# Kernel tuning notes

Measured on AMD Instinct MI355X. Metric: run time of the kernel, lower is better.

## Reference

```python
import jax, jax.numpy as jnp
import numpy as np

N = 50000
E = 800000
HEADS = 4
CH = 64
NEG_SLOPE = 0.2


def _ln(x, g, b, eps=1e-5):
    m = x.mean(-1, keepdims=True)
    v = ((x - m) ** 2).mean(-1, keepdims=True)
    return (x - m) / jnp.sqrt(v + eps) * g + b


def _gat_conv(x, src, dst, W, att_src, att_dst, bias, heads, ch, concat):
    """PyG-style GATConv (self-loops already appended to src/dst)."""
    n = x.shape[0]
    h = (x @ W).reshape(n, heads, ch)                 # [N,H,C]
    a_s = (h * att_src).sum(-1)                        # [N,H]
    a_d = (h * att_dst).sum(-1)                        # [N,H]
    e = jax.nn.leaky_relu(a_s[src] + a_d[dst], NEG_SLOPE)   # [E',H]
    emax = jax.ops.segment_max(e, dst, num_segments=n)      # every node has a self-loop
    ex = jnp.exp(e - emax[dst])
    denom = jax.ops.segment_sum(ex, dst, num_segments=n)
    alpha = ex / (denom[dst] + 1e-16)                  # [E',H]
    out = jax.ops.segment_sum(alpha[:, :, None] * h[src], dst, num_segments=n)  # [N,H,C]
    out = out.reshape(n, heads * ch) if concat else out.mean(axis=1)
    return out + bias


def setup_inputs() -> dict:
    key = jax.random.key(0)
    ks = jax.random.split(key, 32)
    s = 0.05
    inp = {
        "positions": jax.random.normal(ks[0], (N, 3), jnp.float32),
        "degrees": jax.random.uniform(ks[1], (N,), jnp.float32),
        "traffic_info": jax.random.normal(ks[2], (5,), jnp.float32),
        "edge_index": jax.random.randint(ks[3], (2, E), 0, N, jnp.int64),
        # node_encoder: Linear(4,32) + LayerNorm(32)
        "enc_w": jax.random.normal(ks[4], (4, 32), jnp.float32) * s,
        "enc_b": jnp.zeros((32,), jnp.float32),
        "enc_g": jnp.ones((32,), jnp.float32),
        "enc_be": jnp.zeros((32,), jnp.float32),
        # gat1: in=32, out=64, heads=4, concat
        "gat1_w": jax.random.normal(ks[5], (32, HEADS * CH), jnp.float32) * s,
        "gat1_as": jax.random.normal(ks[6], (HEADS, CH), jnp.float32) * s,
        "gat1_ad": jax.random.normal(ks[7], (HEADS, CH), jnp.float32) * s,
        "gat1_b": jnp.zeros((HEADS * CH,), jnp.float32),
        "n1_g": jnp.ones((HEADS * CH,), jnp.float32),
        "n1_b": jnp.zeros((HEADS * CH,), jnp.float32),
        # residual proj Linear(32,64)
        "proj_w": jax.random.normal(ks[8], (32, CH), jnp.float32) * s,
        "proj_b": jnp.zeros((CH,), jnp.float32),
        # gat2: in=256, out=64, heads=1, mean
        "gat2_w": jax.random.normal(ks[9], (HEADS * CH, CH), jnp.float32) * s,
        "gat2_as": jax.random.normal(ks[10], (1, CH), jnp.float32) * s,
        "gat2_ad": jax.random.normal(ks[11], (1, CH), jnp.float32) * s,
        "gat2_b": jnp.zeros((CH,), jnp.float32),
        "n2_g": jnp.ones((CH,), jnp.float32),
        "n2_b": jnp.zeros((CH,), jnp.float32),
        # traffic_encoder Linear(5,32)+LN
        "tr_w": jax.random.normal(ks[12], (5, 32), jnp.float32) * s,
        "tr_b": jnp.zeros((32,), jnp.float32),
        "tr_g": jnp.ones((32,), jnp.float32),
        "tr_be": jnp.zeros((32,), jnp.float32),
        # fusion Linear(96,256)+LN
        "fu_w": jax.random.normal(ks[13], (CH + 32, 256), jnp.float32) * s,
        "fu_b": jnp.zeros((256,), jnp.float32),
        "fu_g": jnp.ones((256,), jnp.float32),
        "fu_be": jnp.zeros((256,), jnp.float32),
    }
    return inp


def reference(positions, degrees, traffic_info, enc_w, enc_b, enc_g, enc_be,
              gat1_w, gat1_as, gat1_ad, gat1_b, n1_g, n1_b, proj_w, proj_b,
              gat2_w, gat2_as, gat2_ad, gat2_b, n2_g, n2_b,
              tr_w, tr_b, tr_g, tr_be, fu_w, fu_b, fu_g, fu_be, edge_index):
    n = positions.shape[0]
    loops = jnp.arange(n, dtype=edge_index.dtype)
    src = jnp.concatenate([edge_index[0], loops])
    dst = jnp.concatenate([edge_index[1], loops])
    # node encoder (dropout in eval mode => identity)
    nf = jnp.concatenate([positions, degrees[:, None]], axis=-1)       # [N,4]
    x = _ln(jax.nn.relu(nf @ enc_w + enc_b), enc_g, enc_be)           # [N,32]
    identity = x @ proj_w + proj_b                                     # [N,64]
    h = _gat_conv(x, src, dst, gat1_w, gat1_as, gat1_ad, gat1_b, HEADS, CH, True)
    h = jax.nn.elu(_ln(h, n1_g, n1_b))                                 # [N,256]
    h = _gat_conv(h, src, dst, gat2_w, gat2_as, gat2_ad, gat2_b, 1, CH, False)
    h = jax.nn.elu(_ln(h, n2_g, n2_b) + identity)                      # [N,64]
    pooled = h.mean(axis=0, keepdims=True)                             # [1,64]
    tf = _ln(jax.nn.relu(traffic_info @ tr_w + tr_b), tr_g, tr_be)[None, :]  # [1,32]
    comb = jnp.concatenate([pooled, tf], axis=-1)                      # [1,96]
    return _ln(jax.nn.relu(comb @ fu_w + fu_b), fu_g, fu_be)           # [1,256]
```

## Files before the change

### kernel.cpp

```cpp
#include <hip/hip_runtime.h>


#define NN 50000
#define EE 800000
#define DMAX 32
#define OVCAP 8192
#define NBLK2 3136
#define ENC_BLOCKS 196
#define NB 196
#define LCAP 20
#define BCAP 8192
#define SPCAP 131072
#define ACHUNK 2048
#define A_BLOCKS 391
#define BSTRIDE 16

typedef unsigned short u16;
typedef unsigned int u32;
typedef __attribute__((ext_vector_type(8))) short bf16x8;
typedef __attribute__((ext_vector_type(4))) float f32x4;

__device__ __forceinline__ float b2f(u16 h) { return __uint_as_float(((u32)h) << 16); }
__device__ __forceinline__ float blo(u32 w) { return __uint_as_float(w << 16); }
__device__ __forceinline__ float bhi(u32 w) { return __uint_as_float(w & 0xFFFF0000u); }
__device__ __forceinline__ u16 f2b(float f) {
    u32 u = __float_as_uint(f);
    u32 r = u + 0x7FFFu + ((u >> 16) & 1u);
    return (u16)(r >> 16);
}
__device__ __forceinline__ int hswz(int row, int u16off) {
    return (row * 256 + u16off) ^ ((row & 7) << 3);
}

template <int BF>
__device__ __forceinline__ float ldf(const void* p, int i) {
    if (BF) return b2f(reinterpret_cast<const u16*>(p)[i]);
    return reinterpret_cast<const float*>(p)[i];
}
template <int I64>
__device__ __forceinline__ int ldidx(const void* p, int i) {
    if (I64) return (int)reinterpret_cast<const long long*>(p)[i];
    return reinterpret_cast<const int*>(p)[i];
}

__device__ __forceinline__ int det_bf(const void* enc_g) {
    return *reinterpret_cast<const u32*>(enc_g) == 0x3F803F80u;
}
__device__ __forceinline__ int det_i64(const void* eidx) {
    const int* e = reinterpret_cast<const int*>(eidx);
    return (e[1] == 0 && e[3] == 0 && e[5] == 0);
}

__device__ __forceinline__ float lrelu(float x) { return x > 0.f ? x : 0.2f * x; }
__device__ __forceinline__ float elu(float x) { return x > 0.f ? x : (__expf(x) - 1.f); }
__device__ __forceinline__ float wsum64(float v) {
#pragma unroll
    for (int off = 1; off < 64; off <<= 1) v += __shfl_xor(v, off, 64);
    return v;
}

template <int BF>
__device__ void swz_body(const void* w1, u16* w1p, int base, int stride) {
    for (int D = base; D < 8192; D += stride) {
        int r = D & 7, ln = (D >> 3) & 63, t = (D >> 9) & 3, h = (D >> 11) & 3;
        int k = (ln >> 4) * 8 + r, c = h * 64 + t * 16 + (ln & 15);
        w1p[D] = BF ? reinterpret_cast<const u16*>(w1)[k * 256 + c]
                    : f2b(reinterpret_cast<const float*>(w1)[k * 256 + c]);
    }
}
template <int BF>
__device__ void swzp_body(const void* pw, u16* pwp, int base, int stride) {
    for (int D = base; D < 2048; D += stride) {
        int r = D & 7, ln = (D >> 3) & 63, t = (D >> 9) & 3;
        int k = (ln >> 4) * 8 + r, c = t * 16 + (ln & 15);
        pwp[D] = BF ? reinterpret_cast<const u16*>(pw)[k * 64 + c]
                    : f2b(reinterpret_cast<const float*>(pw)[k * 64 + c]);
    }
}
template <int BF>
__device__ void swz2s_body(const void* w2, u16* w2p, int base, int stride) {
    for (int D = base; D < 16384; D += stride) {
        int r = D & 7, ln = (D >> 3) & 63, ks = (D >> 9) & 7, t = (D >> 12) & 3;
        int k = ks * 32 + (ln >> 4) * 8 + r, c = t * 16 + (ln & 15);
        w2p[D] = BF ? reinterpret_cast<const u16*>(w2)[k * 64 + c]
                    : f2b(reinterpret_cast<const float*>(w2)[k * 64 + c]);
    }
}
template <int BF>
__device__ void swz2_dots(const void* w2, const void* as2v, const void* ad2v, float* was2p,
                          float* wad2p) {
    int k = threadIdx.x;
    float ss = 0.f, dd = 0.f;
    for (int c = 0; c < 64; c++) {
        float wv = ldf<BF>(w2, k * 64 + c);
        ss = fmaf(wv, ldf<BF>(as2v, c), ss);
        dd = fmaf(wv, ldf<BF>(ad2v, c), dd);
    }
    was2p[k] = ss;
    wad2p[k] = dd;
}
__global__ __launch_bounds__(256) void k_swz(const void* w1, const void* pw, const void* w2,
                                             const void* as2v, const void* ad2v,
                                             const void* enc_g, u16* w1p, u16* pwp, u16* w2p,
                                             float* was2p, float* wad2p) {
    int bf = det_bf(enc_g);
    int bid = blockIdx.x;
    if (bid < 16) {
        int base = bid * 256 + threadIdx.x, stride = 16 * 256;
        if (bf) {
            swz_body<1>(w1, w1p, base, stride);
            swzp_body<1>(pw, pwp, base, stride);
            swz2s_body<1>(w2, w2p, base, stride);
        } else {
            swz_body<0>(w1, w1p, base, stride);
            swzp_body<0>(pw, pwp, base, stride);
            swz2s_body<0>(w2, w2p, base, stride);
        }
    } else {
        if (bf) swz2_dots<1>(w2, as2v, ad2v, was2p, wad2p);
        else swz2_dots<0>(w2, as2v, ad2v, was2p, wad2p);
    }
}

template <int I64>
__device__ void binA_body(const void* eidx, u32* bucket, int* bcnt, int* spill, int* scnt, int sb,
                          u32* lbin, int* bc, int* bbase) {
    for (int b = threadIdx.x; b < NB; b += 256) bc[b] = 0;
    __syncthreads();
    int base = sb * ACHUNK;
#pragma unroll
    for (int j = 0; j < 8; j++) {
        int e = base + j * 256 + threadIdx.x;
        if (e < EE) {
            int s = ldidx<I64>(eidx, e);
            int d = ldidx<I64>(eidx, EE + e);
            int b = d >> 8;
            int p = atomicAdd(&bc[b], 1);
            if (p < LCAP) {
                lbin[b * LCAP + p] = ((u32)(d & 255) << 16) | (u32)s;
            } else {
                int o = atomicAdd(scnt, 1);
                if (o < SPCAP) { spill[2 * o] = d; spill[2 * o + 1] = s; }
            }
        }
    }
    __syncthreads();
    for (int b = threadIdx.x; b < NB; b += 256) {
        int c = bc[b];
        if (c > LCAP) c = LCAP;
        bc[b] = c;
        int cr = (c + 15) & ~15;
        bbase[b] = cr > 0 ? atomicAdd(&bcnt[b * BSTRIDE], cr) : 0;
    }
    __syncthreads();
    int wave = threadIdx.x >> 6, lane = threadIdx.x & 63;
    for (int b = wave; b < NB; b += 4) {
        int c = bc[b], bs = bbase[b];
        int cr = (c + 15) & ~15;
        for (int i = lane; i < cr; i += 64) {
            int pos = bs + i;
            u32 w = (i < c) ? lbin[b * LCAP + i] : 0xFFFF0000u;
            if (pos < BCAP) {
                bucket[(size_t)b * BCAP + pos] = w;
            } else if (i < c) {
                int o = atomicAdd(scnt, 1);
                if (o < SPCAP) {
                    spill[2 * o] = (b << 8) | (int)(w >> 16);
                    spill[2 * o + 1] = (int)(w & 0xFFFFu);
                }
            }
        }
    }
}

template <int BF>
__device__ void enc_body(const void* pos, const void* deg, const void* enc_w, const void* enc_b,
                         const void* enc_g, const void* enc_be, const u16* pwp,
                         const void* proj_b, u16* xo, float* identity, float* a_s1, float* a_d1,
                         const float (*vs)[32], const float (*vd)[32], u32* aggE, int b) {
    int tid = threadIdx.x;
    int n = b * 256 + tid;
    int valid = n < NN;
    float v[32];
#pragma unroll
    for (int c = 0; c < 32; c++) v[c] = 0.f;
    if (valid) {
        float f0 = ldf<BF>(pos, n * 3 + 0), f1 = ldf<BF>(pos, n * 3 + 1);
        float f2 = ldf<BF>(pos, n * 3 + 2), f3 = ldf<BF>(deg, n);
        float s = 0.f, q = 0.f;
#pragma unroll
        for (int c = 0; c < 32; c++) {
            float a = ldf<BF>(enc_b, c) + f0 * ldf<BF>(enc_w, c) + f1 * ldf<BF>(enc_w, 32 + c) +
                      f2 * ldf<BF>(enc_w, 64 + c) + f3 * ldf<BF>(enc_w, 96 + c);
            a = fmaxf(a, 0.f);
            v[c] = a;
            s += a;
            q += a * a;
        }
        float m = s * (1.f / 32.f);
        float rstd = rsqrtf(q * (1.f / 32.f) - m * m + 1e-5f);
#pragma unroll
        for (int c = 0; c < 32; c++) {
            v[c] = (v[c] - m) * rstd * ldf<BF>(enc_g, c) + ldf<BF>(enc_be, c);
            xo[n * 32 + c] = f2b(v[c]);
        }
#pragma unroll
        for (int h = 0; h < 4; h++) {
            float ss = 0.f, dd = 0.f;
#pragma unroll
            for (int k = 0; k < 32; k++) {
                ss = fmaf(v[k], vs[h][k], ss);
                dd = fmaf(v[k], vd[h][k], dd);
            }
            a_s1[n * 4 + h] = ss;
            a_d1[n * 4 + h] = dd;
        }
    }
#pragma unroll
    for (int p = 0; p < 16; p++)
        aggE[tid * 16 + p] = valid ? ((u32)f2b(v[2 * p]) | ((u32)f2b(v[2 * p + 1]) << 16)) : 0u;
    __syncthreads();

    int wave = tid >> 6, lane = tid & 63;
    bf16x8 bf0 = __builtin_bit_cast(bf16x8, *reinterpret_cast<const uint4*>(pwp + ((0 * 64 + lane)) * 8));
    bf16x8 bf1 = __builtin_bit_cast(bf16x8, *reinterpret_cast<const uint4*>(pwp + ((1 * 64 + lane)) * 8));
    bf16x8 bf2 = __builtin_bit_cast(bf16x8, *reinterpret_cast<const uint4*>(pwp + ((2 * 64 + lane)) * 8));
    bf16x8 bf3 = __builtin_bit_cast(bf16x8, *reinterpret_cast<const uint4*>(pwp + ((3 * 64 + lane)) * 8));
    int col = lane & 15;
    float pb0 = ldf<BF>(proj_b, 0 * 16 + col);
    float pb1 = ldf<BF>(proj_b, 1 * 16 + col);
    float pb2 = ldf<BF>(proj_b, 2 * 16 + col);
    float pb3 = ldf<BF>(proj_b, 3 * 16 + col);
    f32x4 z = {0.f, 0.f, 0.f, 0.f};
#pragma unroll
    for (int s = 0; s < 4; s++) {
        int rowbase = wave * 64 + s * 16;
        uint4 au = *reinterpret_cast<const uint4*>(aggE + (rowbase + col) * 16 + (lane >> 4) * 4);
        bf16x8 af = __builtin_bit_cast(bf16x8, au);
        f32x4 c0 = __builtin_amdgcn_mfma_f32_16x16x32_bf16(af, bf0, z, 0, 0, 0);
        f32x4 c1 = __builtin_amdgcn_mfma_f32_16x16x32_bf16(af, bf1, z, 0, 0, 0);
        f32x4 c2 = __builtin_amdgcn_mfma_f32_16x16x32_bf16(af, bf2, z, 0, 0, 0);
        f32x4 c3 = __builtin_amdgcn_mfma_f32_16x16x32_bf16(af, bf3, z, 0, 0, 0);
        int rb2 = (lane >> 4) * 4;
#pragma unroll
        for (int rr = 0; rr < 4; rr++) {
            int node = b * 256 + rowbase + rb2 + rr;
            if (node < NN) {
                identity[(size_t)node * 64 + 0 * 16 + col] = c0[rr] + pb0;
                identity[(size_t)node * 64 + 1 * 16 + col] = c1[rr] + pb1;
                identity[(size_t)node * 64 + 2 * 16 + col] = c2[rr] + pb2;
                identity[(size_t)node * 64 + 3 * 16 + col] = c3[rr] + pb3;
            }
        }
    }
}
template <int BF>
__device__ void enc_pre(const void* w1, const void* asv, const void* adv, float (*vs)[32],
                        float (*vd)[32]) {
    int t = threadIdx.x;
    int h = (t >> 5) & 3, k = t & 31;
    const void* att = (t >> 7) ? adv : asv;
    float s = 0.f;
    for (int c = 0; c < 64; c++)
        s = fmaf(ldf<BF>(w1, k * 256 + h * 64 + c), ldf<BF>(att, h * 64 + c), s);
    if (t >> 7) vd[h][k] = s;
    else vs[h][k] = s;
}
__global__ __launch_bounds__(256) void kAS_bin_enc(
    const void* pos, const void* deg, const void* enc_w, const void* enc_b, const void* enc_g,
    const void* enc_be, const void* proj_b, const void* w1, const void* asv,
    const void* adv, const void* eidx, u16* xo, float* identity, float* a_s1, float* a_d1,
    u32* bucket, int* bcnt, int* spill, int* scnt, const u16* pwp) {
    __shared__ u32 sbuf[4424];
    int bid = blockIdx.x;
    int is_enc = (bid < 2 * ENC_BLOCKS) && ((bid & 1) == 0);
    if (!is_enc) {
        u32* lbin = sbuf;
        int* bc = (int*)(sbuf + NB * LCAP);
        int* bbase = bc + NB;
        int sb = (bid < 2 * ENC_BLOCKS) ? (bid >> 1) : (bid - ENC_BLOCKS);
        if (det_i64(eidx)) binA_body<1>(eidx, bucket, bcnt, spill, scnt, sb, lbin, bc, bbase);
        else binA_body<0>(eidx, bucket, bcnt, spill, scnt, sb, lbin, bc, bbase);
    } else {
        u32* aggE = sbuf;
        float (*vs)[32] = (float(*)[32])(sbuf + 4096);
        float (*vd)[32] = (float(*)[32])(sbuf + 4224);
        int bf = det_bf(enc_g);
        if (bf) enc_pre<1>(w1, asv, adv, vs, vd);
        else enc_pre<0>(w1, asv, adv, vs, vd);
        __syncthreads();
        int b = bid >> 1;
        if (bf)
            enc_body<1>(pos, deg, enc_w, enc_b, enc_g, enc_be, pwp, proj_b, xo, identity, a_s1,
                        a_d1, vs, vd, aggE, b);
        else
            enc_body<0>(pos, deg, enc_w, enc_b, enc_g, enc_be, pwp, proj_b, xo, identity, a_s1,
                        a_d1, vs, vd, aggE, b);
    }
}

__global__ __launch_bounds__(256) void k_csrB(const u32* bucket, const int* bcnt, int* counts,
                                              u16* csr, int* ovlist) {
    __shared__ int lcnt[256];
    int bk = blockIdx.x;
    lcnt[threadIdx.x] = 0;
    __syncthreads();
    int cnt = bcnt[bk * BSTRIDE];
    if (cnt > BCAP) cnt = BCAP;
    const u32* bp = bucket + (size_t)bk * BCAP;
    for (int i = threadIdx.x; i < cnt; i += 256) {
        u32 w = bp[i];
        int dl = w >> 16;
        if (dl >= 256) continue;
        int s = (int)(w & 0xFFFFu);
        int p = atomicAdd(&lcnt[dl], 1);
        int d = (bk << 8) | dl;
        if (p < DMAX) {
            csr[d * DMAX + p] = (u16)s;
        } else {
            int o = atomicAdd(&counts[NN], 1);
            if (o < OVCAP) { ovlist[2 * o] = d; ovlist[2 * o + 1] = s; }
        }
    }
    __syncthreads();
    int node = (bk << 8) | threadIdx.x;
    if (node < NN) counts[node] = lcnt[threadIdx.x];
}

__global__ __launch_bounds__(256) void k_csrC(const int* spill, const int* scnt, int* counts,
                                              u16* csr, int* ovlist) {
    int sc = *scnt;
    if (sc > SPCAP) sc = SPCAP;
    for (int i = threadIdx.x; i < sc; i += 256) {
        int d = spill[2 * i], s = spill[2 * i + 1];
        int p = atomicAdd(&counts[d], 1);
        if (p < DMAX) {
            csr[d * DMAX + p] = (u16)s;
        } else {
            int o = atomicAdd(&counts[NN], 1);
            if (o < OVCAP) { ovlist[2 * o] = d; ovlist[2 * o + 1] = s; }
        }
    }
}

template <int BF>
__device__ void gat1x_body(const u16* x, const float* a_s1, const float* a_d1, const int* counts,
                           const u16* csr, const int* ovlist, const u16* w1p_g, const void* b1,
                           const void* lng, const void* lnb, const u16* w2p_g,
                           const float* was2p, const float* wad2p, u16* h2, float* a_s2,
                           float* a_d2, u32* slds, float* wlds, u32* aggB, float* stats) {
    int wave = threadIdx.x >> 6, lane = threadIdx.x & 63;
    int ns = lane >> 4, t = lane & 15;
    int n = blockIdx.x * 16 + wave * 4 + ns;
    uint4 bfr0 = *reinterpret_cast<const uint4*>(w1p_g + ((wave * 4 + 0) * 64 + lane) * 8);
    uint4 bfr1 = *reinterpret_cast<const uint4*>(w1p_g + ((wave * 4 + 1) * 64 + lane) * 8);
    uint4 bfr2 = *reinterpret_cast<const uint4*>(w1p_g + ((wave * 4 + 2) * 64 + lane) * 8);
    uint4 bfr3 = *reinterpret_cast<const uint4*>(w1p_g + ((wave * 4 + 3) * 64 + lane) * 8);

    float4 ad4 = *reinterpret_cast<const float4*>(a_d1 + n * 4);
    int cnt = counts[n];
    int end = cnt < DMAX ? cnt : DMAX;
    const u16* row = csr + n * DMAX;

    float4 scs = *reinterpret_cast<const float4*>(a_s1 + n * 4);
    float ws0 = __expf(lrelu(scs.x + ad4.x));
    float ws1 = __expf(lrelu(scs.y + ad4.y));
    float ws2 = __expf(lrelu(scs.z + ad4.z));
    float ws3 = __expf(lrelu(scs.w + ad4.w));
    float den0 = ws0, den1 = ws1, den2 = ws2, den3 = ws3;
    u32 xqs = *reinterpret_cast<const u32*>(x + (size_t)n * 32 + t * 2);
    float xs0 = blo(xqs), xs1 = bhi(xqs);
    float a00 = ws0 * xs0, a01 = ws0 * xs1;
    float a10 = ws1 * xs0, a11 = ws1 * xs1;
    float a20 = ws2 * xs0, a21 = ws2 * xs1;
    float a30 = ws3 * xs0, a31 = ws3 * xs1;

    int lbase = wave * 64;
    int npass = __any(end > 16) ? 2 : 1;
    int do4 = __any(end > 24);
    for (int p = 0; p < npass; p++) {
        int e1 = p * 16 + t;
        int valid = e1 < end;
        int s = 0;
        float w0 = 0.f, w1 = 0.f, w2 = 0.f, w3 = 0.f;
        if (valid) {
            s = row[e1];
            float4 sc = *reinterpret_cast<const float4*>(a_s1 + s * 4);
            w0 = __expf(lrelu(sc.x + ad4.x));
            w1 = __expf(lrelu(sc.y + ad4.y));
            w2 = __expf(lrelu(sc.z + ad4.z));
            w3 = __expf(lrelu(sc.w + ad4.w));
        }
        int wi = lbase + t * 4 + ns;
        slds[wi] = (u32)s;
        *reinterpret_cast<float4*>(wlds + wi * 4) = make_float4(w0, w1, w2, w3);
        float d0 = w0, d1 = w1, d2 = w2, d3 = w3;
#pragma unroll
        for (int off = 1; off < 16; off <<= 1) {
            d0 += __shfl_xor(d0, off, 64);
            d1 += __shfl_xor(d1, off, 64);
            d2 += __shfl_xor(d2, off, 64);
            d3 += __shfl_xor(d3, off, 64);
        }
        den0 += d0; den1 += d1; den2 += d2; den3 += d3;
#pragma unroll
        for (int eb = 0; eb < 2; eb++) {
            if (p == 1 && eb == 1 && !do4) continue;
            u32 se0 = slds[lbase + (eb * 8 + 0) * 4 + ns];
            u32 se1 = slds[lbase + (eb * 8 + 1) * 4 + ns];
            u32 se2 = slds[lbase + (eb * 8 + 2) * 4 + ns];
            u32 se3 = slds[lbase + (eb * 8 + 3) * 4 + ns];
            u32 se4 = slds[lbase + (eb * 8 + 4) * 4 + ns];
            u32 se5 = slds[lbase + (eb * 8 + 5) * 4 + ns];
            u32 se6 = slds[lbase + (eb * 8 + 6) * 4 + ns];
            u32 se7 = slds[lbase + (eb * 8 + 7) * 4 + ns];
            u32 xq0 = *reinterpret_cast<const u32*>(x + (size_t)se0 * 32 + t * 2);
            u32 xq1 = *reinterpret_cast<const u32*>(x + (size_t)se1 * 32 + t * 2);
            u32 xq2 = *reinterpret_cast<const u32*>(x + (size_t)se2 * 32 + t * 2);
            u32 xq3 = *reinterpret_cast<const u32*>(x + (size_t)se3 * 32 + t * 2);
            u32 xq4 = *reinterpret_cast<const u32*>(x + (size_t)se4 * 32 + t * 2);
            u32 xq5 = *reinterpret_cast<const u32*>(x + (size_t)se5 * 32 + t * 2);
            u32 xq6 = *reinterpret_cast<const u32*>(x + (size_t)se6 * 32 + t * 2);
            u32 xq7 = *reinterpret_cast<const u32*>(x + (size_t)se7 * 32 + t * 2);
#pragma unroll
            for (int e = 0; e < 8; e++) {
                u32 xq = e == 0 ? xq0 : e == 1 ? xq1 : e == 2 ? xq2 : e == 3 ? xq3
                       : e == 4 ? xq4 : e == 5 ? xq5 : e == 6 ? xq6 : xq7;
                int ri = lbase + (eb * 8 + e) * 4 + ns;
                float4 w4 = *reinterpret_cast<const float4*>(wlds + ri * 4);
                float xv0 = blo(xq), xv1 = bhi(xq);
                a00 = fmaf(w4.x, xv0, a00); a01 = fmaf(w4.x, xv1, a01);
                a10 = fmaf(w4.y, xv0, a10); a11 = fmaf(w4.y, xv1, a11);
                a20 = fmaf(w4.z, xv0, a20); a21 = fmaf(w4.z, xv1, a21);
                a30 = fmaf(w4.w, xv0, a30); a31 = fmaf(w4.w, xv1, a31);
            }
        }
    }
    if (cnt > DMAX) {
        int ovn = counts[NN];
        if (ovn > OVCAP) ovn = OVCAP;
        for (int j = 0; j < ovn; j++) {
            if (ovlist[2 * j] == n) {
                int s = ovlist[2 * j + 1];
                float4 sc = *reinterpret_cast<const float4*>(a_s1 + s * 4);
                u32 xq = *reinterpret_cast<const u32*>(x + (size_t)s * 32 + t * 2);
                float xv0 = blo(xq), xv1 = bhi(xq);
                float w0 = __expf(lrelu(sc.x + ad4.x));
                float w1 = __expf(lrelu(sc.y + ad4.y));
                float w2 = __expf(lrelu(sc.z + ad4.z));
                float w3 = __expf(lrelu(sc.w + ad4.w));
                den0 += w0; den1 += w1; den2 += w2; den3 += w3;
                a00 = fmaf(w0, xv0, a00); a01 = fmaf(w0, xv1, a01);
                a10 = fmaf(w1, xv0, a10); a11 = fmaf(w1, xv1, a11);
                a20 = fmaf(w2, xv0, a20); a21 = fmaf(w2, xv1, a21);
                a30 = fmaf(w3, xv0, a30); a31 = fmaf(w3, xv1, a31);
            }
        }
    }
    float r0 = 1.f / (den0 + 1e-16f);
    float r1 = 1.f / (den1 + 1e-16f);
    float r2 = 1.f / (den2 + 1e-16f);
    float r3 = 1.f / (den3 + 1e-16f);
    int rowi = wave * 4 + ns;
    aggB[(0 * 16 + rowi) * 16 + t] = (u32)f2b(a00 * r0) | ((u32)f2b(a01 * r0) << 16);
    aggB[(1 * 16 + rowi) * 16 + t] = (u32)f2b(a10 * r1) | ((u32)f2b(a11 * r1) << 16);
    aggB[(2 * 16 + rowi) * 16 + t] = (u32)f2b(a20 * r2) | ((u32)f2b(a21 * r2) << 16);
    aggB[(3 * 16 + rowi) * 16 + t] = (u32)f2b(a30 * r3) | ((u32)f2b(a31 * r3) << 16);
    __syncthreads();

    uint4 au = *reinterpret_cast<const uint4*>(aggB + (wave * 16 + (lane & 15)) * 16 +
                                               (lane >> 4) * 4);
    bf16x8 af = __builtin_bit_cast(bf16x8, au);
    f32x4 z = {0.f, 0.f, 0.f, 0.f};
    f32x4 c0 = __builtin_amdgcn_mfma_f32_16x16x32_bf16(af, __builtin_bit_cast(bf16x8, bfr0), z, 0, 0, 0);
    f32x4 c1 = __builtin_amdgcn_mfma_f32_16x16x32_bf16(af, __builtin_bit_cast(bf16x8, bfr1), z, 0, 0, 0);
    f32x4 c2 = __builtin_amdgcn_mfma_f32_16x16x32_bf16(af, __builtin_bit_cast(bf16x8, bfr2), z, 0, 0, 0);
    f32x4 c3 = __builtin_amdgcn_mfma_f32_16x16x32_bf16(af, __builtin_bit_cast(bf16x8, bfr3), z, 0, 0, 0);
    int colc = lane & 15;
    int rbase = (lane >> 4) * 4;
    int cq = wave * 64 + colc;
    float b10 = ldf<BF>(b1, cq), b11 = ldf<BF>(b1, cq + 16);
    float b12 = ldf<BF>(b1, cq + 32), b13 = ldf<BF>(b1, cq + 48);
    float g0 = ldf<BF>(lng, cq), g1 = ldf<BF>(lng, cq + 16);
    float g2 = ldf<BF>(lng, cq + 32), g3 = ldf<BF>(lng, cq + 48);
    float l0 = ldf<BF>(lnb, cq), l1 = ldf<BF>(lnb, cq + 16);
    float l2 = ldf<BF>(lnb, cq + 32), l3 = ldf<BF>(lnb, cq + 48);
    float smp[4], sqp[4];
#pragma unroll
    for (int rr = 0; rr < 4; rr++) {
        float v0 = c0[rr] + b10, v1 = c1[rr] + b11, v2 = c2[rr] + b12, v3 = c3[rr] + b13;
        float sm = (v0 + v1) + (v2 + v3);
        float sq = fmaf(v0, v0, fmaf(v1, v1, fmaf(v2, v2, v3 * v3)));
#pragma unroll
        for (int off = 1; off < 16; off <<= 1) {
            sm += __shfl_xor(sm, off, 64);
            sq += __shfl_xor(sq, off, 64);
        }
        smp[rr] = sm;
        sqp[rr] = sq;
    }
    if (colc == 0) {
#pragma unroll
        for (int rr = 0; rr < 4; rr++) {
            stats[((rbase + rr) * 4 + wave) * 2 + 0] = smp[rr];
            stats[((rbase + rr) * 4 + wave) * 2 + 1] = sqp[rr];
        }
    }
    __syncthreads();
    u16* hb16 = reinterpret_cast<u16*>(slds);
#pragma unroll
    for (int rr = 0; rr < 4; rr++) {
        int rown = rbase + rr;
        float sm = stats[(rown * 4 + 0) * 2] + stats[(rown * 4 + 1) * 2] +
                   stats[(rown * 4 + 2) * 2] + stats[(rown * 4 + 3) * 2];
        float sq = stats[(rown * 4 + 0) * 2 + 1] + stats[(rown * 4 + 1) * 2 + 1] +
                   stats[(rown * 4 + 2) * 2 + 1] + stats[(rown * 4 + 3) * 2 + 1];
        float mm = sm * (1.f / 256.f);
        float rstd = rsqrtf(sq * (1.f / 256.f) - mm * mm + 1e-5f);
        float y0 = elu((c0[rr] + b10 - mm) * rstd * g0 + l0);
        float y1 = elu((c1[rr] + b11 - mm) * rstd * g1 + l1);
        float y2 = elu((c2[rr] + b12 - mm) * rstd * g2 + l2);
        float y3 = elu((c3[rr] + b13 - mm) * rstd * g3 + l3);
        hb16[hswz(rown, cq)]      = f2b(y0);
        hb16[hswz(rown, cq + 16)] = f2b(y1);
        hb16[hswz(rown, cq + 32)] = f2b(y2);
        hb16[hswz(rown, cq + 48)] = f2b(y3);
    }
    __syncthreads();

    f32x4 acc = z;
#pragma unroll
    for (int ks = 0; ks < 8; ks++) {
        bf16x8 bfw = __builtin_bit_cast(
            bf16x8, *reinterpret_cast<const uint4*>(w2p_g + ((wave * 8 + ks) * 64 + lane) * 8));
        bf16x8 afh = __builtin_bit_cast(
            bf16x8,
            *reinterpret_cast<const uint4*>(hb16 + hswz(lane & 15, ks * 32 + (lane >> 4) * 8)));
        acc = __builtin_amdgcn_mfma_f32_16x16x32_bf16(afh, bfw, acc, 0, 0, 0);
    }
    {
        int col2 = wave * 16 + (lane & 15);
        int rb2 = (lane >> 4) * 4;
#pragma unroll
        for (int rr = 0; rr < 4; rr++)
            h2[(size_t)(blockIdx.x * 16 + rb2 + rr) * 64 + col2] = f2b(acc[rr]);
    }
#pragma unroll
    for (int rr = 0; rr < 4; rr++) {
        int ri = wave * 4 + rr;
        uint2 hv = *reinterpret_cast<const uint2*>(hb16 + hswz(ri, lane * 4));
        float y0 = blo(hv.x), y1 = bhi(hv.x), y2 = blo(hv.y), y3 = bhi(hv.y);
        float4 wsv = *reinterpret_cast<const float4*>(was2p + lane * 4);
        float4 wdv = *reinterpret_cast<const float4*>(wad2p + lane * 4);
        float sd = fmaf(y0, wsv.x, fmaf(y1, wsv.y, fmaf(y2, wsv.z, y3 * wsv.w)));
        float dd = fmaf(y0, wdv.x, fmaf(y1, wdv.y, fmaf(y2, wdv.z, y3 * wdv.w)));
        sd = wsum64(sd);
        dd = wsum64(dd);
        if (lane == 0) {
            int n2 = blockIdx.x * 16 + ri;
            a_s2[n2] = sd;
            a_d2[n2] = dd;
        }
    }
}
__global__ __launch_bounds__(256) void k_gat1x(const u16* x, const float* a_s1, const float* a_d1,
                                               const int* counts, const u16* csr,
                                               const int* ovlist, const u16* w1p_g, const void* b1,
                                               const void* lng, const void* lnb,
                                               const u16* w2p_g, const float* was2p,
                                               const float* wad2p, const void* enc_g, u16* h2,
                                               float* a_s2, float* a_d2) {
    __shared__ u32 ubuf[2304];
    __shared__ float stats[128];
    u32* slds = ubuf;
    float* wlds = (float*)(ubuf + 256);
    u32* aggB = ubuf + 1280;
    if (det_bf(enc_g))
        gat1x_body<1>(x, a_s1, a_d1, counts, csr, ovlist, w1p_g, b1, lng, lnb, w2p_g, was2p,
                      wad2p, h2, a_s2, a_d2, slds, wlds, aggB, stats);
    else
        gat1x_body<0>(x, a_s1, a_d1, counts, csr, ovlist, w1p_g, b1, lng, lnb, w2p_g, was2p,
                      wad2p, h2, a_s2, a_d2, slds, wlds, aggB, stats);
}

template <int BF>
__device__ void gat2_body(const u16* h2, const float* a_s2, const float* a_d2, const int* counts,
                          const u16* csr, const int* ovlist, const void* b2, const void* lng,
                          const void* lnb, const float* identity, float* part,
                          u32* swl, float* wwl, float* denl, float* wsl, int* endl, int* cntl,
                          float* sacc) {
    int wave = threadIdx.x >> 6, lane = threadIdx.x & 63;
    int ns = lane >> 4, t = lane & 15;
    int n = blockIdx.x * 16 + wave * 4 + ns;
    int lbase = wave * 128;
    int ws = wave * 4 + ns;

    float ad = 0.f;
    int cnt = 0, end = 0;
    float wself = 0.f;
    const u16* row = csr + (size_t)n * DMAX;
    if (n < NN) {
        ad = a_d2[n];
        cnt = counts[n];
        end = cnt < DMAX ? cnt : DMAX;
        wself = __expf(lrelu(a_s2[n] + ad));
    }
    float den = wself;
    int npass = __any(end > 16) ? 2 : 1;
    for (int p = 0; p < npass; p++) {
        int e1 = p * 16 + t;
        int s = 0;
        float w = 0.f;
        if (n < NN && e1 < end) {
            s = row[e1];
            w = __expf(lrelu(a_s2[s] + ad));
        }
        int wi = lbase + e1 * 4 + ns;
        swl[wi] = (u32)s;
        wwl[wi] = w;
        float d = w;
#pragma unroll
        for (int off = 1; off < 16; off <<= 1) d += __shfl_xor(d, off, 64);
        den += d;
    }
    if (t == 0) { denl[ws] = den; wsl[ws] = wself; endl[ws] = end; cntl[ws] = cnt; }

    float gb = ldf<BF>(b2, lane), gg = ldf<BF>(lng, lane), gl = ldf<BF>(lnb, lane);
    float pacc = 0.f;
#pragma unroll
    for (int ns2 = 0; ns2 < 4; ns2++) {
        int n2 = blockIdx.x * 16 + wave * 4 + ns2;
        if (n2 >= NN) continue;
        int ws2 = wave * 4 + ns2;
        float den2 = denl[ws2];
        float acc = wsl[ws2] * b2f(h2[(size_t)n2 * 64 + lane]);
        int end2 = endl[ws2];
        int e = 0;
        for (; e + 7 < end2; e += 8) {
            u32 s0 = swl[lbase + (e + 0) * 4 + ns2];
            u32 s1 = swl[lbase + (e + 1) * 4 + ns2];
            u32 s2 = swl[lbase + (e + 2) * 4 + ns2];
            u32 s3 = swl[lbase + (e + 3) * 4 + ns2];
            u32 s4 = swl[lbase + (e + 4) * 4 + ns2];
            u32 s5 = swl[lbase + (e + 5) * 4 + ns2];
            u32 s6 = swl[lbase + (e + 6) * 4 + ns2];
            u32 s7 = swl[lbase + (e + 7) * 4 + ns2];
            float v0 = b2f(h2[(size_t)s0 * 64 + lane]);
            float v1 = b2f(h2[(size_t)s1 * 64 + lane]);
            float v2 = b2f(h2[(size_t)s2 * 64 + lane]);
            float v3 = b2f(h2[(size_t)s3 * 64 + lane]);
            float v4 = b2f(h2[(size_t)s4 * 64 + lane]);
            float v5 = b2f(h2[(size_t)s5 * 64 + lane]);
            float v6 = b2f(h2[(size_t)s6 * 64 + lane]);
            float v7 = b2f(h2[(size_t)s7 * 64 + lane]);
            float w0 = wwl[lbase + (e + 0) * 4 + ns2];
            float w1 = wwl[lbase + (e + 1) * 4 + ns2];
            float w2 = wwl[lbase + (e + 2) * 4 + ns2];
            float w3 = wwl[lbase + (e + 3) * 4 + ns2];
            float w4 = wwl[lbase + (e + 4) * 4 + ns2];
            float w5 = wwl[lbase + (e + 5) * 4 + ns2];
            float w6 = wwl[lbase + (e + 6) * 4 + ns2];
            float w7 = wwl[lbase + (e + 7) * 4 + ns2];
            acc = fmaf(w0, v0, acc);
            acc = fmaf(w1, v1, acc);
            acc = fmaf(w2, v2, acc);
            acc = fmaf(w3, v3, acc);
            acc = fmaf(w4, v4, acc);
            acc = fmaf(w5, v5, acc);
            acc = fmaf(w6, v6, acc);
            acc = fmaf(w7, v7, acc);
        }
        for (; e + 3 < end2; e += 4) {
            u32 s0 = swl[lbase + (e + 0) * 4 + ns2];
            u32 s1 = swl[lbase + (e + 1) * 4 + ns2];
            u32 s2 = swl[lbase + (e + 2) * 4 + ns2];
            u32 s3 = swl[lbase + (e + 3) * 4 + ns2];
            float v0 = b2f(h2[(size_t)s0 * 64 + lane]);
            float v1 = b2f(h2[(size_t)s1 * 64 + lane]);
            float v2 = b2f(h2[(size_t)s2 * 64 + lane]);
            float v3 = b2f(h2[(size_t)s3 * 64 + lane]);
            float w0 = wwl[lbase + (e + 0) * 4 + ns2];
            float w1 = wwl[lbase + (e + 1) * 4 + ns2];
            float w2 = wwl[lbase + (e + 2) * 4 + ns2];
            float w3 = wwl[lbase + (e + 3) * 4 + ns2];
            acc = fmaf(w0, v0, acc);
            acc = fmaf(w1, v1, acc);
            acc = fmaf(w2, v2, acc);
            acc = fmaf(w3, v3, acc);
        }
        for (; e < end2; e++) {
            u32 s0 = swl[lbase + e * 4 + ns2];
            float w0 = wwl[lbase + e * 4 + ns2];
            acc = fmaf(w0, b2f(h2[(size_t)s0 * 64 + lane]), acc);
        }
        int cnt2 = cntl[ws2];
        if (cnt2 > DMAX) {
            float adn = a_d2[n2];
            int ovn = counts[NN];
            if (ovn > OVCAP) ovn = OVCAP;
            for (int j = 0; j < ovn; j++) {
                if (ovlist[2 * j] == n2) {
                    int s0 = ovlist[2 * j + 1];
                    float w0 = __expf(lrelu(a_s2[s0] + adn));
                    den2 += w0;
                    acc = fmaf(w0, b2f(h2[(size_t)s0 * 64 + lane]), acc);
                }
            }
        }
        float o = acc / (den2 + 1e-16f) + gb;
        float sm = wsum64(o);
        float sq = wsum64(o * o);
        float m = sm * (1.f / 64.f);
        float rstd = rsqrtf(sq * (1.f / 64.f) - m * m + 1e-5f);
        float y = (o - m) * rstd * gg + gl + identity[(size_t)n2 * 64 + lane];
        pacc += elu(y);
    }
    sacc[threadIdx.x] = pacc;
    __syncthreads();
    if (threadIdx.x < 64) {
        float v = sacc[threadIdx.x] + sacc[threadIdx.x + 64] + sacc[threadIdx.x + 128] +
                  sacc[threadIdx.x + 192];
        part[(size_t)threadIdx.x * NBLK2 + blockIdx.x] = v;
    }
}
__global__ __launch_bounds__(256) void k_gat2(const u16* h2, const float* a_s2, const float* a_d2,
                                              const int* counts, const u16* csr, const int* ovlist,
                                              const void* b2, const void* lng, const void* lnb,
                                              const float* identity, const void* enc_g,
                                              float* part) {
    __shared__ u32 swl[4 * 128];
    __shared__ float wwl[4 * 128];
    __shared__ float denl[16], wsl[16];
    __shared__ int endl[16], cntl[16];
    __shared__ float sacc[256];
    if (det_bf(enc_g))
        gat2_body<1>(h2, a_s2, a_d2, counts, csr, ovlist, b2, lng, lnb, identity, part, swl, wwl,
                     denl, wsl, endl, cntl, sacc);
    else
        gat2_body<0>(h2, a_s2, a_d2, counts, csr, ovlist, b2, lng, lnb, identity, part, swl, wwl,
                     denl, wsl, endl, cntl, sacc);
}

__global__ __launch_bounds__(256) void k_red(const float* part, float* pool) {
    __shared__ float red[256];
    int ch = blockIdx.x;
    const float4* p4 = reinterpret_cast<const float4*>(part + (size_t)ch * NBLK2);
    float s = 0.f;
    for (int j = threadIdx.x; j < NBLK2 / 4; j += 256) {
        float4 v = p4[j];
        s += (v.x + v.y) + (v.z + v.w);
    }
    red[threadIdx.x] = s;
    __syncthreads();
    if (threadIdx.x < 64) {
        float v = red[threadIdx.x] + red[threadIdx.x + 64] + red[threadIdx.x + 128] +
                  red[threadIdx.x + 192];
        v = wsum64(v);
        if (threadIdx.x == 0) pool[ch] = v * (1.0f / NN);
    }
}

template <int BF>
__device__ void final_body(const float* pool, const void* traffic, const void* trw,
                           const void* trb, const void* trg, const void* trbe, const void* fuw,
                           const void* fub, const void* fug, const void* fube, void* out,
                           float* comb, float* red, float* stats) {
    int tid = threadIdx.x;
    if (tid < 64) comb[tid] = pool[tid];
    __syncthreads();
    if (tid < 32) {
        float a = ldf<BF>(trb, tid);
        for (int k = 0; k < 5; k++) a = fmaf(ldf<BF>(traffic, k), ldf<BF>(trw, k * 32 + tid), a);
        red[tid] = fmaxf(a, 0.f);
    }
    __syncthreads();
    if (tid == 0) {
        float s = 0.f, q = 0.f;
        for (int i = 0; i < 32; i++) { s += red[i]; q += red[i] * red[i]; }
        float m = s * (1.f / 32.f);
        stats[0] = m;
        stats[1] = rsqrtf(q * (1.f / 32.f) - m * m + 1e-5f);
    }
    __syncthreads();
    if (tid < 32) comb[64 + tid] = (red[tid] - stats[0]) * stats[1] * ldf<BF>(trg, tid) + ldf<BF>(trbe, tid);
    __syncthreads();
    float a = ldf<BF>(fub, tid);
    for (int k = 0; k < 96; k++) a = fmaf(comb[k], ldf<BF>(fuw, k * 256 + tid), a);
    a = fmaxf(a, 0.f);
    red[tid] = a;
    __syncthreads();
    if (tid == 0) {
        float s = 0.f, q = 0.f;
        for (int i = 0; i < 256; i++) { s += red[i]; q += red[i] * red[i]; }
        float m = s * (1.f / 256.f);
        stats[0] = m;
        stats[1] = rsqrtf(q * (1.f / 256.f) - m * m + 1e-5f);
    }
    __syncthreads();
    float y = (a - stats[0]) * stats[1] * ldf<BF>(fug, tid) + ldf<BF>(fube, tid);
    if (BF) reinterpret_cast<u16*>(out)[tid] = f2b(y);
    else reinterpret_cast<float*>(out)[tid] = y;
}
__global__ void k_final(const float* pool, const void* traffic, const void* trw, const void* trb,
                        const void* trg, const void* trbe, const void* fuw, const void* fub,
                        const void* fug, const void* fube, const void* enc_g, void* out) {
    __shared__ float comb[96];
    __shared__ float red[256];
    __shared__ float stats[2];
    if (det_bf(enc_g))
        final_body<1>(pool, traffic, trw, trb, trg, trbe, fuw, fub, fug, fube, out, comb, red, stats);
    else
        final_body<0>(pool, traffic, trw, trb, trg, trbe, fuw, fub, fug, fube, out, comb, red, stats);
}

extern "C" void kernel_launch(void* const* d_in, const int* in_sizes, int n_in, void* d_out,
                              int out_size, void* d_ws, size_t ws_size, hipStream_t stream) {
    const void* positions = d_in[0];
    const void* degrees = d_in[1];
    const void* traffic = d_in[2];
    const void* eidx = d_in[3];
    const void* enc_w = d_in[4];  const void* enc_b = d_in[5];
    const void* enc_g = d_in[6];  const void* enc_be = d_in[7];
    const void* g1w = d_in[8];    const void* g1as = d_in[9];
    const void* g1ad = d_in[10];  const void* g1b = d_in[11];
    const void* n1g = d_in[12];   const void* n1b = d_in[13];
    const void* pw = d_in[14];    const void* pb = d_in[15];
    const void* g2w = d_in[16];   const void* g2as = d_in[17];
    const void* g2ad = d_in[18];  const void* g2b = d_in[19];
    const void* n2g = d_in[20];   const void* n2b = d_in[21];
    const void* trw = d_in[22];   const void* trb = d_in[23];
    const void* trg = d_in[24];   const void* trbe = d_in[25];
    const void* fuw = d_in[26];   const void* fub = d_in[27];
    const void* fug = d_in[28];   const void* fube = d_in[29];

    char* ws = (char*)d_ws;
    size_t off = 0;
    auto alloc = [&](size_t bytes) -> char* {
        char* p = ws + off;
        off = (off + bytes + 255) & ~(size_t)255;
        return p;
    };
    int* counts = (int*)alloc((size_t)(NN + 1 + NB * BSTRIDE + 64) * 4);
    int* bcnt = counts + NN + 1;
    int* scnt = bcnt + NB * BSTRIDE;
    u16* csr = (u16*)alloc((size_t)NN * DMAX * 2);
    int* ovlist = (int*)alloc((size_t)OVCAP * 2 * 4);
    u32* bucket = (u32*)alloc((size_t)NB * BCAP * 4);
    int* spill = (int*)alloc((size_t)SPCAP * 2 * 4);
    u16* w1p = (u16*)alloc(8192 * 2);
    u16* w2p = (u16*)alloc(16384 * 2);
    u16* pwp = (u16*)alloc(2048 * 2);
    float* was2p = (float*)alloc(256 * 4);
    float* wad2p = (float*)alloc(256 * 4);
    float* a_s1 = (float*)alloc((size_t)NN * 4 * 4);
    float* a_d1 = (float*)alloc((size_t)NN * 4 * 4);
    float* a_s2 = (float*)alloc((size_t)NN * 4);
    float* a_d2 = (float*)alloc((size_t)NN * 4);
    float* identity = (float*)alloc((size_t)NN * 64 * 4);
    float* part = (float*)alloc((size_t)64 * NBLK2 * 4);
    float* pool = (float*)alloc(64 * 4);
    u16* x = (u16*)alloc((size_t)NN * 32 * 2);
    u16* h2 = (u16*)alloc((size_t)NN * 64 * 2);

    hipMemsetAsync(counts, 0, (size_t)(NN + 1 + NB * BSTRIDE + 64) * 4, stream);
    k_swz<<<17, 256, 0, stream>>>(g1w, pw, g2w, g2as, g2ad, enc_g, w1p, pwp, w2p, was2p, wad2p);
    kAS_bin_enc<<<A_BLOCKS + ENC_BLOCKS, 256, 0, stream>>>(
        positions, degrees, enc_w, enc_b, enc_g, enc_be, pb, g1w, g1as, g1ad, eidx, x,
        identity, a_s1, a_d1, bucket, bcnt, spill, scnt, pwp);
    k_csrB<<<NB, 256, 0, stream>>>(bucket, bcnt, counts, csr, ovlist);
    k_csrC<<<1, 256, 0, stream>>>(spill, scnt, counts, csr, ovlist);
    k_gat1x<<<3125, 256, 0, stream>>>(x, a_s1, a_d1, counts, csr, ovlist, w1p, g1b, n1g, n1b,
                                      w2p, was2p, wad2p, enc_g, h2, a_s2, a_d2);
    k_gat2<<<NBLK2, 256, 0, stream>>>(h2, a_s2, a_d2, counts, csr, ovlist, g2b, n2g, n2b, identity,
                                      enc_g, part);
    k_red<<<64, 256, 0, stream>>>(part, pool);
    k_final<<<1, 256, 0, stream>>>(pool, traffic, trw, trb, trg, trbe, fuw, fub, fug, fube, enc_g,
                                   d_out);
}
```

Baseline: 240.4 us.

## Fold weight swizzle into binning kernel and merge spill pass into CSR build

Moves the w1/w2 swizzle and attention-dot precompute into extra blocks of the encoder/binning kernel, leaving only the proj-weight swizzle in a single-block pre-kernel. It also removes the single-block k_csrC kernel: each k_csrB block now scans the whole spill list and inserts the entries that belong to its bucket using shared-memory counters. This cuts kernel launches and serialized single-block work. In exchange, every CSR block rereads the full spill list, and the dispatch order inside the fused kernel changes.

```diff
diff --git a/kernel.cpp b/kernel.cpp
--- a/kernel.cpp
+++ b/kernel.cpp
@@ -14,6 +14,7 @@
 #define ACHUNK 2048
 #define A_BLOCKS 391
 #define BSTRIDE 16
+#define SWZ_BLOCKS 17
 
 typedef unsigned short u16;
 typedef unsigned int u32;
@@ -99,27 +100,9 @@
     was2p[k] = ss;
     wad2p[k] = dd;
 }
-__global__ __launch_bounds__(256) void k_swz(const void* w1, const void* pw, const void* w2,
-                                             const void* as2v, const void* ad2v,
-                                             const void* enc_g, u16* w1p, u16* pwp, u16* w2p,
-                                             float* was2p, float* wad2p) {
-    int bf = det_bf(enc_g);
-    int bid = blockIdx.x;
-    if (bid < 16) {
-        int base = bid * 256 + threadIdx.x, stride = 16 * 256;
-        if (bf) {
-            swz_body<1>(w1, w1p, base, stride);
-            swzp_body<1>(pw, pwp, base, stride);
-            swz2s_body<1>(w2, w2p, base, stride);
-        } else {
-            swz_body<0>(w1, w1p, base, stride);
-            swzp_body<0>(pw, pwp, base, stride);
-            swz2s_body<0>(w2, w2p, base, stride);
-        }
-    } else {
-        if (bf) swz2_dots<1>(w2, as2v, ad2v, was2p, wad2p);
-        else swz2_dots<0>(w2, as2v, ad2v, was2p, wad2p);
-    }
+__global__ __launch_bounds__(256) void k_swz(const void* pw, const void* enc_g, u16* pwp) {
+    if (det_bf(enc_g)) swzp_body<1>(pw, pwp, threadIdx.x, 256);
+    else swzp_body<0>(pw, pwp, threadIdx.x, 256);
 }
 
 template <int I64>
@@ -270,9 +253,29 @@
     const void* pos, const void* deg, const void* enc_w, const void* enc_b, const void* enc_g,
     const void* enc_be, const void* proj_b, const void* w1, const void* asv,
     const void* adv, const void* eidx, u16* xo, float* identity, float* a_s1, float* a_d1,
-    u32* bucket, int* bcnt, int* spill, int* scnt, const u16* pwp) {
+    u32* bucket, int* bcnt, int* spill, int* scnt, const u16* pwp,
+    const void* w2, const void* as2v, const void* ad2v, u16* w1p, u16* w2p,
+    float* was2p, float* wad2p) {
     __shared__ u32 sbuf[4424];
     int bid = blockIdx.x;
+    if (bid >= A_BLOCKS + ENC_BLOCKS) {
+        int sb = bid - (A_BLOCKS + ENC_BLOCKS);
+        int bf = det_bf(enc_g);
+        if (sb < 16) {
+            int base = sb * 256 + threadIdx.x, stride = 16 * 256;
+            if (bf) {
+                swz_body<1>(w1, w1p, base, stride);
+                swz2s_body<1>(w2, w2p, base, stride);
+            } else {
+                swz_body<0>(w1, w1p, base, stride);
+                swz2s_body<0>(w2, w2p, base, stride);
+            }
+        } else {
+            if (bf) swz2_dots<1>(w2, as2v, ad2v, was2p, wad2p);
+            else swz2_dots<0>(w2, as2v, ad2v, was2p, wad2p);
+        }
+        return;
+    }
     int is_enc = (bid < 2 * ENC_BLOCKS) && ((bid & 1) == 0);
     if (!is_enc) {
         u32* lbin = sbuf;
@@ -299,7 +302,8 @@
     }
 }
 
-__global__ __launch_bounds__(256) void k_csrB(const u32* bucket, const int* bcnt, int* counts,
+__global__ __launch_bounds__(256) void k_csrB(const u32* bucket, const int* bcnt,
+                                              const int* spill, const int* scnt, int* counts,
                                               u16* csr, int* ovlist) {
     __shared__ int lcnt[256];
     int bk = blockIdx.x;
@@ -322,18 +326,14 @@
             if (o < OVCAP) { ovlist[2 * o] = d; ovlist[2 * o + 1] = s; }
         }
     }
-    __syncthreads();
-    int node = (bk << 8) | threadIdx.x;
-    if (node < NN) counts[node] = lcnt[threadIdx.x];
-}
-
-__global__ __launch_bounds__(256) void k_csrC(const int* spill, const int* scnt, int* counts,
-                                              u16* csr, int* ovlist) {
     int sc = *scnt;
     if (sc > SPCAP) sc = SPCAP;
     for (int i = threadIdx.x; i < sc; i += 256) {
-        int d = spill[2 * i], s = spill[2 * i + 1];
-        int p = atomicAdd(&counts[d], 1);
+        int d = spill[2 * i];
+        if ((d >> 8) != bk) continue;
+        int s = spill[2 * i + 1];
+        int dl = d & 255;
+        int p = atomicAdd(&lcnt[dl], 1);
         if (p < DMAX) {
             csr[d * DMAX + p] = (u16)s;
         } else {
@@ -341,6 +341,9 @@
             if (o < OVCAP) { ovlist[2 * o] = d; ovlist[2 * o + 1] = s; }
         }
     }
+    __syncthreads();
+    int node = (bk << 8) | threadIdx.x;
+    if (node < NN) counts[node] = lcnt[threadIdx.x];
 }
 
 template <int BF>
@@ -863,12 +866,12 @@
     u16* h2 = (u16*)alloc((size_t)NN * 64 * 2);
 
     hipMemsetAsync(counts, 0, (size_t)(NN + 1 + NB * BSTRIDE + 64) * 4, stream);
-    k_swz<<<17, 256, 0, stream>>>(g1w, pw, g2w, g2as, g2ad, enc_g, w1p, pwp, w2p, was2p, wad2p);
-    kAS_bin_enc<<<A_BLOCKS + ENC_BLOCKS, 256, 0, stream>>>(
+    k_swz<<<1, 256, 0, stream>>>(pw, enc_g, pwp);
+    kAS_bin_enc<<<A_BLOCKS + ENC_BLOCKS + SWZ_BLOCKS, 256, 0, stream>>>(
         positions, degrees, enc_w, enc_b, enc_g, enc_be, pb, g1w, g1as, g1ad, eidx, x,
-        identity, a_s1, a_d1, bucket, bcnt, spill, scnt, pwp);
-    k_csrB<<<NB, 256, 0, stream>>>(bucket, bcnt, counts, csr, ovlist);
-    k_csrC<<<1, 256, 0, stream>>>(spill, scnt, counts, csr, ovlist);
+        identity, a_s1, a_d1, bucket, bcnt, spill, scnt, pwp,
+        g2w, g2as, g2ad, w1p, w2p, was2p, wad2p);
+    k_csrB<<<NB, 256, 0, stream>>>(bucket, bcnt, spill, scnt, counts, csr, ovlist);
     k_gat1x<<<3125, 256, 0, stream>>>(x, a_s1, a_d1, counts, csr, ovlist, w1p, g1b, n1g, n1b,
                                       w2p, was2p, wad2p, enc_g, h2, a_s2, a_d2);
     k_gat2<<<NBLK2, 256, 0, stream>>>(h2, a_s2, a_d2, counts, csr, ovlist, g2b, n2g, n2b, identity,
```

Result: no change. 237.2 us (-1.3%).
